# Performance work log

Hardware: AMD Instinct MI355X
Metric: run time of the kernel (lower is better)

The kernel has to match this reference:

```python
import jax, jax.numpy as jnp
import numpy as np

NUM_HEADS = 8
NUM_CONNECTIONS = 4
LOCAL_RADIUS = 1
SPATIAL_SIGMA = 32.0
TEMPORAL_SIGMA = 2.0
SCORER_PATCH_SIZE = (2, 7, 7)  # default used inside compute_proximity_scores
DENSITY_WEIGHT = 1.0
PROXIMITY_WEIGHT = 1.0
NEG = -1e9


def _local_window_mask(N: int, radius: int) -> np.ndarray:
    """Replicates compute_sparse_attention_mask's local-window loop (static)."""
    g = int(np.sqrt(N))
    d = np.arange(-radius, radius + 1)
    dt, dh, dw = np.meshgrid(d, d, d, indexing='ij')
    offsets = (dt * g * g + dh * g + dw).reshape(-1)  # (27,)
    i = np.arange(N)[:, None]
    j = i + offsets[None, :]
    valid = (j >= 0) & (j < N)
    mask = np.zeros((N, N), dtype=bool)
    mask[np.broadcast_to(i, j.shape)[valid], j[valid]] = True
    return mask


def _patch_positions(nT, nH, nW, bt, bh, bw):
    t_idx = np.arange(nT) * bt + bt // 2
    h_idx = np.arange(nH) * bh + bh // 2
    w_idx = np.arange(nW) * bw + bw // 2
    pos = np.stack(np.meshgrid(t_idx, h_idx, w_idx, indexing='ij'), axis=-1)
    return jnp.asarray(pos.reshape(-1, 3), dtype=jnp.float32)  # (N, 3)


def setup_inputs() -> dict:
    key = jax.random.key(0)
    k1, k2, k3 = jax.random.split(key, 3)
    B, T, H, W, C = 1, 4, 28, 28, 256
    x = jax.random.normal(k1, (B, T, H, W, C), dtype=jnp.float32)
    w_qkv = jax.random.normal(k2, (3 * C, C), dtype=jnp.float32) * 0.02
    w_proj = jax.random.normal(k3, (C, C), dtype=jnp.float32) * 0.02
    b_proj = jnp.zeros((C,), dtype=jnp.float32)
    return {"x": x, "w_qkv": w_qkv, "w_proj": w_proj, "b_proj": b_proj,
            "bt": 2, "bh": 7, "bw": 7}


def reference(x, w_qkv, w_proj, b_proj, bt, bh, bw):
    B, T, H, W, C = x.shape
    nT, nH, nW = T // bt, H // bh, W // bw
    N, V = nT * nH * nW, bt * bh * bw
    L = N * V
    hd = C // NUM_HEADS

    # ---- rearrange into patches: b (nt t)(nh h)(nw w) c -> b N V c ----
    patches = x.reshape(B, nT, bt, nH, bh, nW, bw, C)
    patches = patches.transpose(0, 1, 3, 5, 2, 4, 6, 7).reshape(B, N, V, C)

    # ---- density scores (B, N) ----
    dens = jnp.linalg.norm(patches, axis=-1).mean(axis=-1)
    dens = dens / (dens.max(axis=1, keepdims=True) + 1e-8)

    # ---- proximity scores (N, N) ----
    pos = _patch_positions(nT, nH, nW, bt, bh, bw)
    pT, pH, pW = SCORER_PATCH_SIZE
    t_dist = jnp.abs(pos[:, 0:1] - pos[:, 0:1].T) * pT
    h_dist = jnp.abs(pos[:, 1:2] - pos[:, 1:2].T) * pH
    w_dist = jnp.abs(pos[:, 2:3] - pos[:, 2:3].T) * pW
    spatial = jnp.sqrt(h_dist ** 2 + w_dist ** 2)
    prox = jnp.exp(-spatial / SPATIAL_SIGMA) * jnp.exp(-t_dist / TEMPORAL_SIGMA)

    # ---- combined scores (B, N, N) ----
    geo = jnp.sqrt(dens[:, :, None] * dens[:, None, :] + 1e-8)
    scores = DENSITY_WEIGHT * geo + PROXIMITY_WEIGHT * prox[None]

    # ---- sparse attention mask (N, N) ----
    s = scores.mean(0)
    mask = jnp.asarray(_local_window_mask(N, LOCAL_RADIUS))
    k = min(NUM_CONNECTIONS, N - 1)
    s_nodiag = jnp.where(jnp.eye(N, dtype=bool), -jnp.inf, s)
    _, topk_idx = jax.lax.top_k(s_nodiag, k)  # indices: no gradient path
    mask = mask.at[jnp.arange(N)[:, None], topk_idx].set(True)

    # expand block mask to token-level (L, L)
    tmask = jnp.repeat(jnp.repeat(mask, V, axis=0), V, axis=1)

    # ---- block-sparse attention over tokens (dense masked emulation) ----
    tokens = patches.reshape(B, L, C)
    qkv = tokens @ w_qkv.T  # (B, L, 3C)
    q, kk, v = jnp.split(qkv, 3, axis=-1)

    def to_heads(t):
        return t.reshape(B, L, NUM_HEADS, hd).transpose(0, 2, 1, 3)

    q, kk, v = to_heads(q), to_heads(kk), to_heads(v)
    att = jnp.einsum('bhid,bhjd->bhij', q, kk) * (hd ** -0.5)
    att = jnp.where(tmask[None, None], att, NEG)
    att = jax.nn.softmax(att, axis=-1)
    o = jnp.einsum('bhij,bhjd->bhid', att, v)
    o = o.transpose(0, 2, 1, 3).reshape(B, L, C)
    o = o @ w_proj.T + b_proj

    # ---- inverse rearrange back to (B, T, H, W, C) ----
    o = o.reshape(B, nT, nH, nW, bt, bh, bw, C)
    out = o.transpose(0, 1, 4, 2, 5, 3, 6, 7).reshape(B, T, H, W, C)
    return out
```

## Files before the change

### kernel.cpp

```cpp
#include <hip/hip_runtime.h>
#include <hip/hip_bf16.h>
#include <math.h>

#define L_TOK 3136
#define NPATCH 32
#define VTOK 98
#define PADV 128
#define CDIM 256
#define NHEADS 8
#define HD 32

typedef __attribute__((ext_vector_type(8))) short short8;
typedef __attribute__((ext_vector_type(4))) short short4v;
typedef __attribute__((ext_vector_type(4))) float floatx4;

union PU { unsigned u[2]; short4v s; };

static __device__ __forceinline__ unsigned short bf16u(float f) {
    __hip_bfloat16 h = __float2bfloat16(f);
    return *reinterpret_cast<unsigned short*>(&h);
}
static __device__ __forceinline__ float bf16f(unsigned short u) {
    unsigned v = ((unsigned)u) << 16;
    return __uint_as_float(v);
}
static __device__ __forceinline__ void bf16pair(float v, unsigned short& hi, unsigned short& lo) {
    unsigned short h = bf16u(v);
    lo = bf16u(v - bf16f(h));
    hi = h;
}
static __device__ __forceinline__ short8 ldcvt(const float* p) {
    float4 a = *(const float4*)p;
    float4 b = *(const float4*)(p + 4);
    short8 r;
    r[0] = (short)bf16u(a.x); r[1] = (short)bf16u(a.y);
    r[2] = (short)bf16u(a.z); r[3] = (short)bf16u(a.w);
    r[4] = (short)bf16u(b.x); r[5] = (short)bf16u(b.y);
    r[6] = (short)bf16u(b.z); r[7] = (short)bf16u(b.w);
    return r;
}

static __device__ __forceinline__ int token_offset(int l) {
    int pn = l / VTOK, pv = l % VTOK;
    int it = pn >> 4, ih = (pn >> 2) & 3, iw = pn & 3;
    int tt = pv / 49, r2 = pv % 49, hh = r2 / 7, ww = r2 % 7;
    return (((it * 2 + tt) * 28 + ih * 7 + hh) * 28 + iw * 7 + ww) * CDIM;
}

__global__ __launch_bounds__(256) void qkv_density(const float* __restrict__ x,
                                                   const float* __restrict__ wqkv,
                                                   unsigned short* __restrict__ qb,
                                                   unsigned short* __restrict__ kb,
                                                   unsigned short* __restrict__ vt,
                                                   float* __restrict__ dens) {
    __shared__ int rowpn[64];
    __shared__ int rowpv[64];
    __shared__ float wsum[4];
    int tid = threadIdx.x;

    if (blockIdx.y == 12) {
        if (blockIdx.x >= NPATCH) return;
        int n = blockIdx.x;
        int wid = tid >> 6, lane = tid & 63;
        float accn = 0.f;
        for (int v = wid; v < VTOK; v += 4) {
            int off = token_offset(n * VTOK + v);
            float4 xx = *(const float4*)(x + off + lane * 4);
            float ss = xx.x * xx.x + xx.y * xx.y + xx.z * xx.z + xx.w * xx.w;
            #pragma unroll
            for (int o = 32; o > 0; o >>= 1) ss += __shfl_down(ss, o, 64);
            if (lane == 0) accn += sqrtf(ss);
        }
        if (lane == 0) wsum[wid] = accn;
        __syncthreads();
        if (tid == 0) dens[n] = (wsum[0] + wsum[1] + wsum[2] + wsum[3]) * (1.0f / 98.0f);
        return;
    }

    int m0 = blockIdx.x * 64;
    int n0 = blockIdx.y * 64;
    if (tid < 64) {
        int l = m0 + tid;
        rowpn[tid] = l / VTOK;
        rowpv[tid] = l % VTOK;
    }
    __syncthreads();
    const int wave = tid >> 6, lane = tid & 63;
    const int l16 = lane & 15, quad = lane >> 4;
    const int wm = wave & 1, wn = wave >> 1;

    int r0 = m0 + wm * 32 + l16;
    int aoff0 = token_offset(r0);
    int aoff1 = token_offset(r0 + 16);
    int boff0 = (n0 + wn * 32 + l16) * CDIM;
    int boff1 = boff0 + 16 * CDIM;

    const floatx4 zerov = {0.f, 0.f, 0.f, 0.f};
    floatx4 acc[2][2] = {{zerov, zerov}, {zerov, zerov}};
    #pragma unroll
    for (int k0 = 0; k0 < CDIM; k0 += 32) {
        int kk = k0 + quad * 8;
        short8 a0 = ldcvt(x + aoff0 + kk);
        short8 a1 = ldcvt(x + aoff1 + kk);
        short8 b0 = ldcvt(wqkv + boff0 + kk);
        short8 b1 = ldcvt(wqkv + boff1 + kk);
        acc[0][0] = __builtin_amdgcn_mfma_f32_16x16x32_bf16(a0, b0, acc[0][0], 0, 0, 0);
        acc[0][1] = __builtin_amdgcn_mfma_f32_16x16x32_bf16(a0, b1, acc[0][1], 0, 0, 0);
        acc[1][0] = __builtin_amdgcn_mfma_f32_16x16x32_bf16(a1, b0, acc[1][0], 0, 0, 0);
        acc[1][1] = __builtin_amdgcn_mfma_f32_16x16x32_bf16(a1, b1, acc[1][1], 0, 0, 0);
    }

    const float sc = 0.17677669529663689f;
    #pragma unroll
    for (int mt = 0; mt < 2; ++mt) {
        #pragma unroll
        for (int nt = 0; nt < 2; ++nt) {
            int col = n0 + wn * 32 + nt * 16 + l16;
            #pragma unroll
            for (int r = 0; r < 4; ++r) {
                int mrow = wm * 32 + mt * 16 + quad * 4 + r;
                int pn = rowpn[mrow], vv = rowpv[mrow];
                float val = acc[mt][nt][r];
                if (col < 256) {
                    qb[(size_t)(pn * PADV + vv) * CDIM + col] = bf16u(val * sc);
                } else if (col < 512) {
                    kb[(size_t)(pn * PADV + vv) * CDIM + (col - 256)] = bf16u(val);
                } else {
                    vt[(size_t)pn * (CDIM * PADV) + (col - 512) * PADV + vv] = bf16u(val);
                }
            }
        }
    }
}

__global__ __launch_bounds__(256) void attn_mfma(const unsigned short* __restrict__ qb,
                                                 const unsigned short* __restrict__ kb,
                                                 const unsigned short* __restrict__ vt,
                                                 const float* __restrict__ dens,
                                                 unsigned short* __restrict__ ohi,
                                                 unsigned short* __restrict__ olo) {
    __shared__ floatx4 ldsO[4][7][2][64];
    __shared__ float   ldsL[4][7][64];
    const int i = blockIdx.x, h = blockIdx.y;
    const int tid = threadIdx.x;
    const int wave = tid >> 6, lane = tid & 63;
    const int l16 = lane & 15, quad = lane >> 4;

    unsigned maskbits;
    {
        int j = lane & 31;
        float dj = dens[j];
        float m = dj;
        #pragma unroll
        for (int o = 16; o > 0; o >>= 1) m = fmaxf(m, __shfl_xor(m, o, 64));
        float inv = 1.0f / (m + 1e-8f);
        float dni = dens[i] * inv, dnj = dj * inv;
        int it_i = i >> 4, ih_i = (i >> 2) & 3, iw_i = i & 3;
        int it_j = j >> 4, ih_j = (j >> 2) & 3, iw_j = j & 3;
        float t_dist = fabsf((float)(2 * (it_i - it_j))) * 2.0f;
        float h_dist = fabsf((float)(7 * (ih_i - ih_j))) * 7.0f;
        float w_dist = fabsf((float)(7 * (iw_i - iw_j))) * 7.0f;
        float spatial = sqrtf(h_dist * h_dist + w_dist * w_dist);
        float prox = expf(-spatial / 32.0f) * expf(-t_dist / 2.0f);
        float val = (j == i) ? -1e30f : (sqrtf(dni * dnj + 1e-8f) + prox);
        unsigned picked = 0;
        #pragma unroll
        for (int t = 0; t < 4; ++t) {
            float best = val;
            #pragma unroll
            for (int o = 16; o > 0; o >>= 1) best = fmaxf(best, __shfl_xor(best, o, 64));
            unsigned long long b = __ballot(val == best);
            int bj = (__ffsll((long long)b) - 1) & 31;
            picked |= 1u << bj;
            if ((lane & 31) == bj) val = -1e30f;
        }
        int delta = j - i;
        bool inwin = false;
        #pragma unroll
        for (int dt = -1; dt <= 1; ++dt)
            #pragma unroll
            for (int dh = -1; dh <= 1; ++dh)
                #pragma unroll
                for (int dw = -1; dw <= 1; ++dw)
                    inwin = inwin || (delta == dt * 25 + dh * 5 + dw);
        unsigned wmask = (unsigned)(__ballot(inwin) & 0xFFFFFFFFull);
        maskbits = wmask | picked;
    }

    short8 Qf[7];
    #pragma unroll
    for (int t = 0; t < 7; ++t)
        Qf[t] = *(const short8*)(qb + (size_t)(i * PADV + t * 16 + l16) * CDIM + h * HD + quad * 8);

    const floatx4 zerov = {0.f, 0.f, 0.f, 0.f};
    floatx4 O[7][2];
    float lsum[7];
    #pragma unroll
    for (int t = 0; t < 7; ++t) { O[t][0] = zerov; O[t][1] = zerov; lsum[t] = 0.f; }

    unsigned bits = maskbits;
    int rank = 0;
    while (bits) {
        int j = __ffs(bits) - 1;
        bits &= bits - 1;
        if ((rank++ & 3) != wave) continue;
        const unsigned short* kbase = kb + (size_t)(j * PADV) * CDIM + h * HD;
        const unsigned short* vbase = vt + (size_t)j * (CDIM * PADV) + (h * HD) * PADV;
        #pragma unroll
        for (int c = 0; c < 7; ++c) {
            short8 Kf = *(const short8*)(kbase + (c * 16 + l16) * CDIM + quad * 8);
            short4v Vf0 = *(const short4v*)(vbase + l16 * PADV + c * 16 + quad * 4);
            short4v Vf1 = *(const short4v*)(vbase + (16 + l16) * PADV + c * 16 + quad * 4);
            #pragma unroll
            for (int t = 0; t < 7; ++t) {
                floatx4 S = __builtin_amdgcn_mfma_f32_16x16x32_bf16(Kf, Qf[t], zerov, 0, 0, 0);
                unsigned up[4];
                #pragma unroll
                for (int r = 0; r < 4; ++r) {
                    float e = __expf(S[r]);
                    if (c == 6 && !(quad == 0 && r < 2)) e = 0.f;
                    unsigned ue = __float_as_uint(e) & 0xFFFF0000u;
                    up[r] = ue;
                    lsum[t] += __uint_as_float(ue);
                }
                PU pu;
                pu.u[0] = __builtin_amdgcn_perm(up[1], up[0], 0x07060302u);
                pu.u[1] = __builtin_amdgcn_perm(up[3], up[2], 0x07060302u);
                O[t][0] = __builtin_amdgcn_mfma_f32_16x16x16bf16_1k(pu.s, Vf0, O[t][0], 0, 0, 0);
                O[t][1] = __builtin_amdgcn_mfma_f32_16x16x16bf16_1k(pu.s, Vf1, O[t][1], 0, 0, 0);
            }
        }
    }

    #pragma unroll
    for (int t = 0; t < 7; ++t) {
        ldsO[wave][t][0][lane] = O[t][0];
        ldsO[wave][t][1][lane] = O[t][1];
        ldsL[wave][t][lane] = lsum[t];
    }
    __syncthreads();
    for (int u = wave; u < 14; u += 4) {
        int t = u >> 1, half = u & 1;
        floatx4 Os = ldsO[0][t][half][lane] + ldsO[1][t][half][lane]
                   + ldsO[2][t][half][lane] + ldsO[3][t][half][lane];
        float Ls = ldsL[0][t][lane] + ldsL[1][t][lane] + ldsL[2][t][lane] + ldsL[3][t][lane];
        Ls += __shfl_xor(Ls, 16, 64);
        Ls += __shfl_xor(Ls, 32, 64);
        #pragma unroll
        for (int r = 0; r < 4; ++r) {
            int q = t * 16 + quad * 4 + r;
            float lv = __shfl(Ls, quad * 4 + r);
            if (q < VTOK) {
                float invl = 1.0f / lv;
                float v = Os[r] * invl;
                unsigned short hi, lo;
                bf16pair(v, hi, lo);
                size_t base = (size_t)(i * VTOK + q) * CDIM + h * HD + half * 16;
                ohi[base + l16] = hi;
                olo[base + l16] = lo;
            }
        }
    }
}

__global__ __launch_bounds__(256) void proj_gemm(const unsigned short* __restrict__ ohi,
                                                 const unsigned short* __restrict__ olo,
                                                 const float* __restrict__ wproj,
                                                 const float* __restrict__ bp,
                                                 float* __restrict__ out) {
    __shared__ int rowoff[64];
    __shared__ __align__(16) unsigned short Bh[32][264];
    __shared__ __align__(16) unsigned short Bl[32][264];
    int tid = threadIdx.x;
    int m0 = blockIdx.x * 64;
    int n0 = blockIdx.y * 32;
    if (tid < 64) rowoff[tid] = token_offset(m0 + tid);
    #pragma unroll
    for (int rep = 0; rep < 8; ++rep) {
        int flat = rep * 256 + tid;
        int row = flat >> 6;
        int c4 = (flat & 63) * 4;
        float4 v = *(const float4*)(wproj + (size_t)(n0 + row) * CDIM + c4);
        ushort4 uh, ul;
        bf16pair(v.x, uh.x, ul.x); bf16pair(v.y, uh.y, ul.y);
        bf16pair(v.z, uh.z, ul.z); bf16pair(v.w, uh.w, ul.w);
        *(ushort4*)(&Bh[row][c4]) = uh;
        *(ushort4*)(&Bl[row][c4]) = ul;
    }
    __syncthreads();

    const int wave = tid >> 6, lane = tid & 63;
    const int l16 = lane & 15, quad = lane >> 4;

    size_t arow = (size_t)(m0 + wave * 16 + l16) * CDIM + quad * 8;

    const floatx4 zerov = {0.f, 0.f, 0.f, 0.f};
    floatx4 acc[2] = {zerov, zerov};
    #pragma unroll 2
    for (int k0 = 0; k0 < CDIM; k0 += 32) {
        int kk = k0 + quad * 8;
        short8 ah = *(const short8*)(ohi + arow + k0);
        short8 al = *(const short8*)(olo + arow + k0);
        short8 bh0 = *(const short8*)(&Bh[l16][kk]);
        short8 bh1 = *(const short8*)(&Bh[16 + l16][kk]);
        short8 bl0 = *(const short8*)(&Bl[l16][kk]);
        short8 bl1 = *(const short8*)(&Bl[16 + l16][kk]);
        acc[0] = __builtin_amdgcn_mfma_f32_16x16x32_bf16(al, bh0, acc[0], 0, 0, 0);
        acc[0] = __builtin_amdgcn_mfma_f32_16x16x32_bf16(ah, bl0, acc[0], 0, 0, 0);
        acc[0] = __builtin_amdgcn_mfma_f32_16x16x32_bf16(ah, bh0, acc[0], 0, 0, 0);
        acc[1] = __builtin_amdgcn_mfma_f32_16x16x32_bf16(al, bh1, acc[1], 0, 0, 0);
        acc[1] = __builtin_amdgcn_mfma_f32_16x16x32_bf16(ah, bl1, acc[1], 0, 0, 0);
        acc[1] = __builtin_amdgcn_mfma_f32_16x16x32_bf16(ah, bh1, acc[1], 0, 0, 0);
    }

    #pragma unroll
    for (int nt = 0; nt < 2; ++nt) {
        int col = n0 + nt * 16 + l16;
        float bias = bp[col];
        #pragma unroll
        for (int r = 0; r < 4; ++r) {
            int mrow = wave * 16 + quad * 4 + r;
            out[rowoff[mrow] + col] = acc[nt][r] + bias;
        }
    }
}

extern "C" void kernel_launch(void* const* d_in, const int* in_sizes, int n_in,
                              void* d_out, int out_size, void* d_ws, size_t ws_size,
                              hipStream_t stream) {
    const float* x      = (const float*)d_in[0];
    const float* w_qkv  = (const float*)d_in[1];
    const float* w_proj = (const float*)d_in[2];
    const float* b_proj = (const float*)d_in[3];
    float* out = (float*)d_out;

    unsigned short* qb  = (unsigned short*)d_ws;
    unsigned short* kb  = qb  + (size_t)NPATCH * PADV * CDIM;
    unsigned short* vt  = kb  + (size_t)NPATCH * PADV * CDIM;
    unsigned short* ohi = vt  + (size_t)NPATCH * PADV * CDIM;
    unsigned short* olo = ohi + (size_t)L_TOK * CDIM;
    float* dens = (float*)(olo + (size_t)L_TOK * CDIM);

    qkv_density<<<dim3(49, 13), 256, 0, stream>>>(x, w_qkv, qb, kb, vt, dens);
    attn_mfma<<<dim3(NPATCH, NHEADS), 256, 0, stream>>>(qb, kb, vt, dens, ohi, olo);
    proj_gemm<<<dim3(49, 8), 256, 0, stream>>>(ohi, olo, w_proj, b_proj, out);
}
```

Baseline: 119.8 us.

## Fuse attention and projection into one kernel with a software grid barrier

Merges the attention and output-projection kernels into one 256-block launch. A global atomic barrier separates the two phases, and the first 196 blocks then run the projection GEMM with wider 64-column tiles. The goal is to drop one kernel launch and its inter-kernel gap. The barrier needs all 256 blocks to be co-resident, which the large LDS footprint could threaten, and its magic-value reset scheme is fragile across repeated calls. The QKV loop unroll is also reduced to 2.

```diff
diff --git a/kernel.cpp b/kernel.cpp
--- a/kernel.cpp
+++ b/kernel.cpp
@@ -9,6 +9,7 @@
 #define CDIM 256
 #define NHEADS 8
 #define HD 32
+#define BAR_MAGIC 0x5EEDF00Du
 
 typedef __attribute__((ext_vector_type(8))) short short8;
 typedef __attribute__((ext_vector_type(4))) short short4v;
@@ -97,7 +98,7 @@
 
     const floatx4 zerov = {0.f, 0.f, 0.f, 0.f};
     floatx4 acc[2][2] = {{zerov, zerov}, {zerov, zerov}};
-    #pragma unroll
+    #pragma unroll 2
     for (int k0 = 0; k0 < CDIM; k0 += 32) {
         int kk = k0 + quad * 8;
         short8 a0 = ldcvt(x + aoff0 + kk);
@@ -133,194 +134,214 @@
     }
 }
 
-__global__ __launch_bounds__(256) void attn_mfma(const unsigned short* __restrict__ qb,
+#define LDSBYTES 66304
+__global__ __launch_bounds__(256) void attn_proj(const unsigned short* __restrict__ qb,
                                                  const unsigned short* __restrict__ kb,
                                                  const unsigned short* __restrict__ vt,
                                                  const float* __restrict__ dens,
                                                  unsigned short* __restrict__ ohi,
-                                                 unsigned short* __restrict__ olo) {
-    __shared__ floatx4 ldsO[4][7][2][64];
-    __shared__ float   ldsL[4][7][64];
-    const int i = blockIdx.x, h = blockIdx.y;
+                                                 unsigned short* __restrict__ olo,
+                                                 const float* __restrict__ wproj,
+                                                 const float* __restrict__ bp,
+                                                 float* __restrict__ out,
+                                                 unsigned* __restrict__ bar) {
+    __shared__ __align__(16) char ldsbuf[LDSBYTES];
     const int tid = threadIdx.x;
     const int wave = tid >> 6, lane = tid & 63;
     const int l16 = lane & 15, quad = lane >> 4;
 
-    unsigned maskbits;
+    if (blockIdx.x == 0 && tid == 0) {
+        bar[1] = 0u; bar[2] = 0u;
+        __threadfence();
+        atomicExch(&bar[0], BAR_MAGIC);
+    }
+
     {
-        int j = lane & 31;
-        float dj = dens[j];
-        float m = dj;
-        #pragma unroll
-        for (int o = 16; o > 0; o >>= 1) m = fmaxf(m, __shfl_xor(m, o, 64));
-        float inv = 1.0f / (m + 1e-8f);
-        float dni = dens[i] * inv, dnj = dj * inv;
-        int it_i = i >> 4, ih_i = (i >> 2) & 3, iw_i = i & 3;
-        int it_j = j >> 4, ih_j = (j >> 2) & 3, iw_j = j & 3;
-        float t_dist = fabsf((float)(2 * (it_i - it_j))) * 2.0f;
-        float h_dist = fabsf((float)(7 * (ih_i - ih_j))) * 7.0f;
-        float w_dist = fabsf((float)(7 * (iw_i - iw_j))) * 7.0f;
-        float spatial = sqrtf(h_dist * h_dist + w_dist * w_dist);
-        float prox = expf(-spatial / 32.0f) * expf(-t_dist / 2.0f);
-        float val = (j == i) ? -1e30f : (sqrtf(dni * dnj + 1e-8f) + prox);
-        unsigned picked = 0;
-        #pragma unroll
-        for (int t = 0; t < 4; ++t) {
-            float best = val;
-            #pragma unroll
-            for (int o = 16; o > 0; o >>= 1) best = fmaxf(best, __shfl_xor(best, o, 64));
-            unsigned long long b = __ballot(val == best);
-            int bj = (__ffsll((long long)b) - 1) & 31;
-            picked |= 1u << bj;
-            if ((lane & 31) == bj) val = -1e30f;
-        }
-        int delta = j - i;
-        bool inwin = false;
-        #pragma unroll
-        for (int dt = -1; dt <= 1; ++dt)
-            #pragma unroll
-            for (int dh = -1; dh <= 1; ++dh)
+        const int i = blockIdx.x >> 3, h = blockIdx.x & 7;
+        floatx4 (*ldsO)[7][2][64] = (floatx4 (*)[7][2][64])ldsbuf;
+        float   (*ldsL)[7][64]    = (float (*)[7][64])(ldsbuf + 57344);
+
+        unsigned maskbits;
+        {
+            int j = lane & 31;
+            float dj = dens[j];
+            float m = dj;
+            #pragma unroll
+            for (int o = 16; o > 0; o >>= 1) m = fmaxf(m, __shfl_xor(m, o, 64));
+            float inv = 1.0f / (m + 1e-8f);
+            float dni = dens[i] * inv, dnj = dj * inv;
+            int it_i = i >> 4, ih_i = (i >> 2) & 3, iw_i = i & 3;
+            int it_j = j >> 4, ih_j = (j >> 2) & 3, iw_j = j & 3;
+            float t_dist = fabsf((float)(2 * (it_i - it_j))) * 2.0f;
+            float h_dist = fabsf((float)(7 * (ih_i - ih_j))) * 7.0f;
+            float w_dist = fabsf((float)(7 * (iw_i - iw_j))) * 7.0f;
+            float spatial = sqrtf(h_dist * h_dist + w_dist * w_dist);
+            float prox = expf(-spatial / 32.0f) * expf(-t_dist / 2.0f);
+            float val = (j == i) ? -1e30f : (sqrtf(dni * dnj + 1e-8f) + prox);
+            unsigned picked = 0;
+            #pragma unroll
+            for (int t = 0; t < 4; ++t) {
+                float best = val;
                 #pragma unroll
-                for (int dw = -1; dw <= 1; ++dw)
-                    inwin = inwin || (delta == dt * 25 + dh * 5 + dw);
-        unsigned wmask = (unsigned)(__ballot(inwin) & 0xFFFFFFFFull);
-        maskbits = wmask | picked;
-    }
-
-    short8 Qf[7];
-    #pragma unroll
-    for (int t = 0; t < 7; ++t)
-        Qf[t] = *(const short8*)(qb + (size_t)(i * PADV + t * 16 + l16) * CDIM + h * HD + quad * 8);
-
-    const floatx4 zerov = {0.f, 0.f, 0.f, 0.f};
-    floatx4 O[7][2];
-    float lsum[7];
-    #pragma unroll
-    for (int t = 0; t < 7; ++t) { O[t][0] = zerov; O[t][1] = zerov; lsum[t] = 0.f; }
-
-    unsigned bits = maskbits;
-    int rank = 0;
-    while (bits) {
-        int j = __ffs(bits) - 1;
-        bits &= bits - 1;
-        if ((rank++ & 3) != wave) continue;
-        const unsigned short* kbase = kb + (size_t)(j * PADV) * CDIM + h * HD;
-        const unsigned short* vbase = vt + (size_t)j * (CDIM * PADV) + (h * HD) * PADV;
-        #pragma unroll
-        for (int c = 0; c < 7; ++c) {
-            short8 Kf = *(const short8*)(kbase + (c * 16 + l16) * CDIM + quad * 8);
-            short4v Vf0 = *(const short4v*)(vbase + l16 * PADV + c * 16 + quad * 4);
-            short4v Vf1 = *(const short4v*)(vbase + (16 + l16) * PADV + c * 16 + quad * 4);
-            #pragma unroll
-            for (int t = 0; t < 7; ++t) {
-                floatx4 S = __builtin_amdgcn_mfma_f32_16x16x32_bf16(Kf, Qf[t], zerov, 0, 0, 0);
-                unsigned up[4];
+                for (int o = 16; o > 0; o >>= 1) best = fmaxf(best, __shfl_xor(best, o, 64));
+                unsigned long long b = __ballot(val == best);
+                int bj = (__ffsll((long long)b) - 1) & 31;
+                picked |= 1u << bj;
+                if ((lane & 31) == bj) val = -1e30f;
+            }
+            int delta = j - i;
+            bool inwin = false;
+            #pragma unroll
+            for (int dt = -1; dt <= 1; ++dt)
                 #pragma unroll
-                for (int r = 0; r < 4; ++r) {
-                    float e = __expf(S[r]);
-                    if (c == 6 && !(quad == 0 && r < 2)) e = 0.f;
-                    unsigned ue = __float_as_uint(e) & 0xFFFF0000u;
-                    up[r] = ue;
-                    lsum[t] += __uint_as_float(ue);
+                for (int dh = -1; dh <= 1; ++dh)
+                    #pragma unroll
+                    for (int dw = -1; dw <= 1; ++dw)
+                        inwin = inwin || (delta == dt * 25 + dh * 5 + dw);
+            unsigned wmask = (unsigned)(__ballot(inwin) & 0xFFFFFFFFull);
+            maskbits = wmask | picked;
+        }
+
+        short8 Qf[7];
+        #pragma unroll
+        for (int t = 0; t < 7; ++t)
+            Qf[t] = *(const short8*)(qb + (size_t)(i * PADV + t * 16 + l16) * CDIM + h * HD + quad * 8);
+
+        const floatx4 zerov = {0.f, 0.f, 0.f, 0.f};
+        floatx4 O[7][2];
+        float lsum[7];
+        #pragma unroll
+        for (int t = 0; t < 7; ++t) { O[t][0] = zerov; O[t][1] = zerov; lsum[t] = 0.f; }
+
+        unsigned bits = maskbits;
+        int rank = 0;
+        while (bits) {
+            int j = __ffs(bits) - 1;
+            bits &= bits - 1;
+            if ((rank++ & 3) != wave) continue;
+            const unsigned short* kbase = kb + (size_t)(j * PADV) * CDIM + h * HD;
+            const unsigned short* vbase = vt + (size_t)j * (CDIM * PADV) + (h * HD) * PADV;
+            #pragma unroll
+            for (int c = 0; c < 7; ++c) {
+                short8 Kf = *(const short8*)(kbase + (c * 16 + l16) * CDIM + quad * 8);
+                short4v Vf0 = *(const short4v*)(vbase + l16 * PADV + c * 16 + quad * 4);
+                short4v Vf1 = *(const short4v*)(vbase + (16 + l16) * PADV + c * 16 + quad * 4);
+                #pragma unroll
+                for (int t = 0; t < 7; ++t) {
+                    floatx4 S = __builtin_amdgcn_mfma_f32_16x16x32_bf16(Kf, Qf[t], zerov, 0, 0, 0);
+                    unsigned up[4];
+                    #pragma unroll
+                    for (int r = 0; r < 4; ++r) {
+                        float e = __expf(S[r]);
+                        if (c == 6 && !(quad == 0 && r < 2)) e = 0.f;
+                        unsigned ue = __float_as_uint(e) & 0xFFFF0000u;
+                        up[r] = ue;
+                        lsum[t] += __uint_as_float(ue);
+                    }
+                    PU pu;
+                    pu.u[0] = __builtin_amdgcn_perm(up[1], up[0], 0x07060302u);
+                    pu.u[1] = __builtin_amdgcn_perm(up[3], up[2], 0x07060302u);
+                    O[t][0] = __builtin_amdgcn_mfma_f32_16x16x16bf16_1k(pu.s, Vf0, O[t][0], 0, 0, 0);
+                    O[t][1] = __builtin_amdgcn_mfma_f32_16x16x16bf16_1k(pu.s, Vf1, O[t][1], 0, 0, 0);
                 }
-                PU pu;
-                pu.u[0] = __builtin_amdgcn_perm(up[1], up[0], 0x07060302u);
-                pu.u[1] = __builtin_amdgcn_perm(up[3], up[2], 0x07060302u);
-                O[t][0] = __builtin_amdgcn_mfma_f32_16x16x16bf16_1k(pu.s, Vf0, O[t][0], 0, 0, 0);
-                O[t][1] = __builtin_amdgcn_mfma_f32_16x16x16bf16_1k(pu.s, Vf1, O[t][1], 0, 0, 0);
-            }
-        }
-    }
-
-    #pragma unroll
-    for (int t = 0; t < 7; ++t) {
-        ldsO[wave][t][0][lane] = O[t][0];
-        ldsO[wave][t][1][lane] = O[t][1];
-        ldsL[wave][t][lane] = lsum[t];
-    }
+            }
+        }
+
+        #pragma unroll
+        for (int t = 0; t < 7; ++t) {
+            ldsO[wave][t][0][lane] = O[t][0];
+            ldsO[wave][t][1][lane] = O[t][1];
+            ldsL[wave][t][lane] = lsum[t];
+        }
+        __syncthreads();
+        for (int u = wave; u < 14; u += 4) {
+            int t = u >> 1, half = u & 1;
+            floatx4 Os = ldsO[0][t][half][lane] + ldsO[1][t][half][lane]
+                       + ldsO[2][t][half][lane] + ldsO[3][t][half][lane];
+            float Ls = ldsL[0][t][lane] + ldsL[1][t][lane] + ldsL[2][t][lane] + ldsL[3][t][lane];
+            Ls += __shfl_xor(Ls, 16, 64);
+            Ls += __shfl_xor(Ls, 32, 64);
+            #pragma unroll
+            for (int r = 0; r < 4; ++r) {
+                int q = t * 16 + quad * 4 + r;
+                float lv = __shfl(Ls, quad * 4 + r);
+                if (q < VTOK) {
+                    float invl = 1.0f / lv;
+                    float v = Os[r] * invl;
+                    unsigned short hi, lo;
+                    bf16pair(v, hi, lo);
+                    size_t base = (size_t)(i * VTOK + q) * CDIM + h * HD + half * 16;
+                    ohi[base + l16] = hi;
+                    olo[base + l16] = lo;
+                }
+            }
+        }
+    }
+
+    __threadfence();
     __syncthreads();
-    for (int u = wave; u < 14; u += 4) {
-        int t = u >> 1, half = u & 1;
-        floatx4 Os = ldsO[0][t][half][lane] + ldsO[1][t][half][lane]
-                   + ldsO[2][t][half][lane] + ldsO[3][t][half][lane];
-        float Ls = ldsL[0][t][lane] + ldsL[1][t][lane] + ldsL[2][t][lane] + ldsL[3][t][lane];
-        Ls += __shfl_xor(Ls, 16, 64);
-        Ls += __shfl_xor(Ls, 32, 64);
-        #pragma unroll
-        for (int r = 0; r < 4; ++r) {
-            int q = t * 16 + quad * 4 + r;
-            float lv = __shfl(Ls, quad * 4 + r);
-            if (q < VTOK) {
-                float invl = 1.0f / lv;
-                float v = Os[r] * invl;
-                unsigned short hi, lo;
-                bf16pair(v, hi, lo);
-                size_t base = (size_t)(i * VTOK + q) * CDIM + h * HD + half * 16;
-                ohi[base + l16] = hi;
-                olo[base + l16] = lo;
-            }
-        }
-    }
-}
-
-__global__ __launch_bounds__(256) void proj_gemm(const unsigned short* __restrict__ ohi,
-                                                 const unsigned short* __restrict__ olo,
-                                                 const float* __restrict__ wproj,
-                                                 const float* __restrict__ bp,
-                                                 float* __restrict__ out) {
-    __shared__ int rowoff[64];
-    __shared__ __align__(16) unsigned short Bh[32][264];
-    __shared__ __align__(16) unsigned short Bl[32][264];
-    int tid = threadIdx.x;
-    int m0 = blockIdx.x * 64;
-    int n0 = blockIdx.y * 32;
-    if (tid < 64) rowoff[tid] = token_offset(m0 + tid);
-    #pragma unroll
-    for (int rep = 0; rep < 8; ++rep) {
-        int flat = rep * 256 + tid;
-        int row = flat >> 6;
-        int c4 = (flat & 63) * 4;
-        float4 v = *(const float4*)(wproj + (size_t)(n0 + row) * CDIM + c4);
-        ushort4 uh, ul;
-        bf16pair(v.x, uh.x, ul.x); bf16pair(v.y, uh.y, ul.y);
-        bf16pair(v.z, uh.z, ul.z); bf16pair(v.w, uh.w, ul.w);
-        *(ushort4*)(&Bh[row][c4]) = uh;
-        *(ushort4*)(&Bl[row][c4]) = ul;
+    if (tid == 0) {
+        while (atomicAdd(&bar[0], 0u) != BAR_MAGIC) __builtin_amdgcn_s_sleep(2);
+        unsigned a = atomicAdd(&bar[1], 1u);
+        if (a == (unsigned)(gridDim.x - 1)) {
+            atomicExch(&bar[2], 1u);
+        } else {
+            while (atomicAdd(&bar[2], 0u) == 0u) __builtin_amdgcn_s_sleep(2);
+        }
     }
     __syncthreads();
-
-    const int wave = tid >> 6, lane = tid & 63;
-    const int l16 = lane & 15, quad = lane >> 4;
-
-    size_t arow = (size_t)(m0 + wave * 16 + l16) * CDIM + quad * 8;
-
-    const floatx4 zerov = {0.f, 0.f, 0.f, 0.f};
-    floatx4 acc[2] = {zerov, zerov};
-    #pragma unroll 2
-    for (int k0 = 0; k0 < CDIM; k0 += 32) {
-        int kk = k0 + quad * 8;
-        short8 ah = *(const short8*)(ohi + arow + k0);
-        short8 al = *(const short8*)(olo + arow + k0);
-        short8 bh0 = *(const short8*)(&Bh[l16][kk]);
-        short8 bh1 = *(const short8*)(&Bh[16 + l16][kk]);
-        short8 bl0 = *(const short8*)(&Bl[l16][kk]);
-        short8 bl1 = *(const short8*)(&Bl[16 + l16][kk]);
-        acc[0] = __builtin_amdgcn_mfma_f32_16x16x32_bf16(al, bh0, acc[0], 0, 0, 0);
-        acc[0] = __builtin_amdgcn_mfma_f32_16x16x32_bf16(ah, bl0, acc[0], 0, 0, 0);
-        acc[0] = __builtin_amdgcn_mfma_f32_16x16x32_bf16(ah, bh0, acc[0], 0, 0, 0);
-        acc[1] = __builtin_amdgcn_mfma_f32_16x16x32_bf16(al, bh1, acc[1], 0, 0, 0);
-        acc[1] = __builtin_amdgcn_mfma_f32_16x16x32_bf16(ah, bl1, acc[1], 0, 0, 0);
-        acc[1] = __builtin_amdgcn_mfma_f32_16x16x32_bf16(ah, bh1, acc[1], 0, 0, 0);
-    }
-
-    #pragma unroll
-    for (int nt = 0; nt < 2; ++nt) {
-        int col = n0 + nt * 16 + l16;
-        float bias = bp[col];
-        #pragma unroll
-        for (int r = 0; r < 4; ++r) {
-            int mrow = wave * 16 + quad * 4 + r;
-            out[rowoff[mrow] + col] = acc[nt][r] + bias;
+    __threadfence();
+
+    if (blockIdx.x >= 196) return;
+    {
+        int m0 = (blockIdx.x % 49) * 64;
+        int n0 = (blockIdx.x / 49) * 64;
+        int* rowoff = (int*)ldsbuf;
+        unsigned short (*Bh)[258] = (unsigned short (*)[258])(ldsbuf + 256);
+        unsigned short (*Bl)[258] = (unsigned short (*)[258])(ldsbuf + 256 + 33024);
+
+        if (tid < 64) rowoff[tid] = token_offset(m0 + tid);
+        #pragma unroll
+        for (int rep = 0; rep < 16; ++rep) {
+            int flat = rep * 256 + tid;
+            int row = flat >> 6;
+            int c4 = (flat & 63) * 4;
+            float4 v = *(const float4*)(wproj + (size_t)(n0 + row) * CDIM + c4);
+            ushort4 uh, ul;
+            bf16pair(v.x, uh.x, ul.x); bf16pair(v.y, uh.y, ul.y);
+            bf16pair(v.z, uh.z, ul.z); bf16pair(v.w, uh.w, ul.w);
+            *(ushort4*)(&Bh[row][c4]) = uh;
+            *(ushort4*)(&Bl[row][c4]) = ul;
+        }
+        __syncthreads();
+
+        size_t arow = (size_t)(m0 + wave * 16 + l16) * CDIM + quad * 8;
+        const floatx4 zerov = {0.f, 0.f, 0.f, 0.f};
+        floatx4 acc[4] = {zerov, zerov, zerov, zerov};
+        #pragma unroll 2
+        for (int k0 = 0; k0 < CDIM; k0 += 32) {
+            int kk = k0 + quad * 8;
+            short8 ah = *(const short8*)(ohi + arow + k0);
+            short8 al = *(const short8*)(olo + arow + k0);
+            #pragma unroll
+            for (int nt = 0; nt < 4; ++nt) {
+                short8 bh = *(const short8*)(&Bh[nt * 16 + l16][kk]);
+                short8 bl = *(const short8*)(&Bl[nt * 16 + l16][kk]);
+                acc[nt] = __builtin_amdgcn_mfma_f32_16x16x32_bf16(al, bh, acc[nt], 0, 0, 0);
+                acc[nt] = __builtin_amdgcn_mfma_f32_16x16x32_bf16(ah, bl, acc[nt], 0, 0, 0);
+                acc[nt] = __builtin_amdgcn_mfma_f32_16x16x32_bf16(ah, bh, acc[nt], 0, 0, 0);
+            }
+        }
+
+        #pragma unroll
+        for (int nt = 0; nt < 4; ++nt) {
+            int col = n0 + nt * 16 + l16;
+            float bias = bp[col];
+            #pragma unroll
+            for (int r = 0; r < 4; ++r) {
+                int mrow = wave * 16 + quad * 4 + r;
+                out[rowoff[mrow] + col] = acc[nt][r] + bias;
+            }
         }
     }
 }
@@ -340,8 +361,8 @@
     unsigned short* ohi = vt  + (size_t)NPATCH * PADV * CDIM;
     unsigned short* olo = ohi + (size_t)L_TOK * CDIM;
     float* dens = (float*)(olo + (size_t)L_TOK * CDIM);
+    unsigned* bar = (unsigned*)(dens + NPATCH);
 
     qkv_density<<<dim3(49, 13), 256, 0, stream>>>(x, w_qkv, qb, kb, vt, dens);
-    attn_mfma<<<dim3(NPATCH, NHEADS), 256, 0, stream>>>(qb, kb, vt, dens, ohi, olo);
-    proj_gemm<<<dim3(49, 8), 256, 0, stream>>>(ohi, olo, w_proj, b_proj, out);
-}
+    attn_proj<<<256, 256, 0, stream>>>(qb, kb, vt, dens, ohi, olo, w_proj, b_proj, out, bar);
+}
```

Measured after the change: 178.4 us. 48.9% more time.

## Stage QKV output through LDS, store V row-major, use 8 waves in attention

Applied to the files above, without the earlier changes.

The QKV epilogue now writes bf16 results into an LDS tile and then emits coalesced 16-byte row stores for Q, K and V. V is kept row-major instead of transposed, which removes the strided scatter of the V^T writes. The attention kernel reads V with per-row 32-bit loads and repacks them into MFMA operands with perm instructions. It also runs 8 waves per block instead of 4, splitting the neighbour patches across more waves and adding a two-stage LDS reduction. The costs are extra V load instructions and more register pressure per block, and the QKV k-loop is now only partly unrolled.

```diff
diff --git a/kernel.cpp b/kernel.cpp
--- a/kernel.cpp
+++ b/kernel.cpp
@@ -51,11 +51,12 @@
                                                    const float* __restrict__ wqkv,
                                                    unsigned short* __restrict__ qb,
                                                    unsigned short* __restrict__ kb,
-                                                   unsigned short* __restrict__ vt,
+                                                   unsigned short* __restrict__ vb,
                                                    float* __restrict__ dens) {
     __shared__ int rowpn[64];
     __shared__ int rowpv[64];
     __shared__ float wsum[4];
+    __shared__ __align__(16) unsigned short Ct[64][72];
     int tid = threadIdx.x;
 
     if (blockIdx.y == 12) {
@@ -97,7 +98,7 @@
 
     const floatx4 zerov = {0.f, 0.f, 0.f, 0.f};
     floatx4 acc[2][2] = {{zerov, zerov}, {zerov, zerov}};
-    #pragma unroll
+    #pragma unroll 2
     for (int k0 = 0; k0 < CDIM; k0 += 32) {
         int kk = k0 + quad * 8;
         short8 a0 = ldcvt(x + aoff0 + kk);
@@ -110,32 +111,31 @@
         acc[1][1] = __builtin_amdgcn_mfma_f32_16x16x32_bf16(a1, b1, acc[1][1], 0, 0, 0);
     }
 
-    const float sc = 0.17677669529663689f;
-    #pragma unroll
-    for (int mt = 0; mt < 2; ++mt) {
-        #pragma unroll
-        for (int nt = 0; nt < 2; ++nt) {
-            int col = n0 + wn * 32 + nt * 16 + l16;
-            #pragma unroll
-            for (int r = 0; r < 4; ++r) {
-                int mrow = wm * 32 + mt * 16 + quad * 4 + r;
-                int pn = rowpn[mrow], vv = rowpv[mrow];
-                float val = acc[mt][nt][r];
-                if (col < 256) {
-                    qb[(size_t)(pn * PADV + vv) * CDIM + col] = bf16u(val * sc);
-                } else if (col < 512) {
-                    kb[(size_t)(pn * PADV + vv) * CDIM + (col - 256)] = bf16u(val);
-                } else {
-                    vt[(size_t)pn * (CDIM * PADV) + (col - 512) * PADV + vv] = bf16u(val);
-                }
-            }
-        }
-    }
-}
-
-__global__ __launch_bounds__(256) void attn_mfma(const unsigned short* __restrict__ qb,
+    const int ytype = blockIdx.y >> 2;
+    const float sc = (ytype == 0) ? 0.17677669529663689f : 1.0f;
+    #pragma unroll
+    for (int mt = 0; mt < 2; ++mt)
+        #pragma unroll
+        for (int nt = 0; nt < 2; ++nt)
+            #pragma unroll
+            for (int r = 0; r < 4; ++r)
+                Ct[wm * 32 + mt * 16 + quad * 4 + r][wn * 32 + nt * 16 + l16] =
+                    bf16u(acc[mt][nt][r] * sc);
+    __syncthreads();
+    unsigned short* ob = (ytype == 0) ? qb : (ytype == 1) ? kb : vb;
+    int nlocal0 = (blockIdx.y & 3) * 64;
+    #pragma unroll
+    for (int it = 0; it < 2; ++it) {
+        int idx = it * 256 + tid;
+        int row = idx >> 3, chunk = idx & 7;
+        short8 cv = *(const short8*)(&Ct[row][chunk * 8]);
+        *(short8*)(ob + (size_t)(rowpn[row] * PADV + rowpv[row]) * CDIM + nlocal0 + chunk * 8) = cv;
+    }
+}
+
+__global__ __launch_bounds__(512) void attn_mfma(const unsigned short* __restrict__ qb,
                                                  const unsigned short* __restrict__ kb,
-                                                 const unsigned short* __restrict__ vt,
+                                                 const unsigned short* __restrict__ vb,
                                                  const float* __restrict__ dens,
                                                  unsigned short* __restrict__ ohi,
                                                  unsigned short* __restrict__ olo) {
@@ -203,14 +203,21 @@
     while (bits) {
         int j = __ffs(bits) - 1;
         bits &= bits - 1;
-        if ((rank++ & 3) != wave) continue;
+        if ((rank++ & 7) != wave) continue;
         const unsigned short* kbase = kb + (size_t)(j * PADV) * CDIM + h * HD;
-        const unsigned short* vbase = vt + (size_t)j * (CDIM * PADV) + (h * HD) * PADV;
+        const unsigned short* vbase = vb + (size_t)(j * PADV) * CDIM + h * HD + 2 * l16;
         #pragma unroll
         for (int c = 0; c < 7; ++c) {
             short8 Kf = *(const short8*)(kbase + (c * 16 + l16) * CDIM + quad * 8);
-            short4v Vf0 = *(const short4v*)(vbase + l16 * PADV + c * 16 + quad * 4);
-            short4v Vf1 = *(const short4v*)(vbase + (16 + l16) * PADV + c * 16 + quad * 4);
+            unsigned w0 = *(const unsigned*)(vbase + (c * 16 + quad * 4 + 0) * CDIM);
+            unsigned w1 = *(const unsigned*)(vbase + (c * 16 + quad * 4 + 1) * CDIM);
+            unsigned w2 = *(const unsigned*)(vbase + (c * 16 + quad * 4 + 2) * CDIM);
+            unsigned w3 = *(const unsigned*)(vbase + (c * 16 + quad * 4 + 3) * CDIM);
+            PU vf0, vf1;
+            vf0.u[0] = __builtin_amdgcn_perm(w1, w0, 0x05040100u);
+            vf0.u[1] = __builtin_amdgcn_perm(w3, w2, 0x05040100u);
+            vf1.u[0] = __builtin_amdgcn_perm(w1, w0, 0x07060302u);
+            vf1.u[1] = __builtin_amdgcn_perm(w3, w2, 0x07060302u);
             #pragma unroll
             for (int t = 0; t < 7; ++t) {
                 floatx4 S = __builtin_amdgcn_mfma_f32_16x16x32_bf16(Kf, Qf[t], zerov, 0, 0, 0);
@@ -226,23 +233,40 @@
                 PU pu;
                 pu.u[0] = __builtin_amdgcn_perm(up[1], up[0], 0x07060302u);
                 pu.u[1] = __builtin_amdgcn_perm(up[3], up[2], 0x07060302u);
-                O[t][0] = __builtin_amdgcn_mfma_f32_16x16x16bf16_1k(pu.s, Vf0, O[t][0], 0, 0, 0);
-                O[t][1] = __builtin_amdgcn_mfma_f32_16x16x16bf16_1k(pu.s, Vf1, O[t][1], 0, 0, 0);
+                O[t][0] = __builtin_amdgcn_mfma_f32_16x16x16bf16_1k(pu.s, vf0.s, O[t][0], 0, 0, 0);
+                O[t][1] = __builtin_amdgcn_mfma_f32_16x16x16bf16_1k(pu.s, vf1.s, O[t][1], 0, 0, 0);
             }
         }
     }
 
-    #pragma unroll
-    for (int t = 0; t < 7; ++t) {
-        ldsO[wave][t][0][lane] = O[t][0];
-        ldsO[wave][t][1][lane] = O[t][1];
-        ldsL[wave][t][lane] = lsum[t];
-    }
-    __syncthreads();
-    for (int u = wave; u < 14; u += 4) {
-        int t = u >> 1, half = u & 1;
-        floatx4 Os = ldsO[0][t][half][lane] + ldsO[1][t][half][lane]
-                   + ldsO[2][t][half][lane] + ldsO[3][t][half][lane];
+    if (wave >= 4) {
+        int s = wave - 4;
+        #pragma unroll
+        for (int t = 0; t < 7; ++t) {
+            ldsO[s][t][0][lane] = O[t][0];
+            ldsO[s][t][1][lane] = O[t][1];
+            ldsL[s][t][lane] = lsum[t];
+        }
+    }
+    __syncthreads();
+    if (wave < 4) {
+        #pragma unroll
+        for (int t = 0; t < 7; ++t) {
+            O[t][0] += ldsO[wave][t][0][lane];
+            O[t][1] += ldsO[wave][t][1][lane];
+            lsum[t] += ldsL[wave][t][lane];
+            ldsO[wave][t][0][lane] = O[t][0];
+            ldsO[wave][t][1][lane] = O[t][1];
+            ldsL[wave][t][lane] = lsum[t];
+        }
+    }
+    __syncthreads();
+    if (wave < 7) {
+        int t = wave;
+        floatx4 Os0 = ldsO[0][t][0][lane] + ldsO[1][t][0][lane]
+                    + ldsO[2][t][0][lane] + ldsO[3][t][0][lane];
+        floatx4 Os1 = ldsO[0][t][1][lane] + ldsO[1][t][1][lane]
+                    + ldsO[2][t][1][lane] + ldsO[3][t][1][lane];
         float Ls = ldsL[0][t][lane] + ldsL[1][t][lane] + ldsL[2][t][lane] + ldsL[3][t][lane];
         Ls += __shfl_xor(Ls, 16, 64);
         Ls += __shfl_xor(Ls, 32, 64);
@@ -252,12 +276,13 @@
             float lv = __shfl(Ls, quad * 4 + r);
             if (q < VTOK) {
                 float invl = 1.0f / lv;
-                float v = Os[r] * invl;
-                unsigned short hi, lo;
-                bf16pair(v, hi, lo);
-                size_t base = (size_t)(i * VTOK + q) * CDIM + h * HD + half * 16;
-                ohi[base + l16] = hi;
-                olo[base + l16] = lo;
+                float v0 = Os0[r] * invl, v1 = Os1[r] * invl;
+                unsigned short h0, g0, h1, g1;
+                bf16pair(v0, h0, g0);
+                bf16pair(v1, h1, g1);
+                size_t base = (size_t)(i * VTOK + q) * CDIM + h * HD + 2 * l16;
+                *(unsigned*)(ohi + base) = (unsigned)h0 | ((unsigned)h1 << 16);
+                *(unsigned*)(olo + base) = (unsigned)g0 | ((unsigned)g1 << 16);
             }
         }
     }
@@ -336,12 +361,12 @@
 
     unsigned short* qb  = (unsigned short*)d_ws;
     unsigned short* kb  = qb  + (size_t)NPATCH * PADV * CDIM;
-    unsigned short* vt  = kb  + (size_t)NPATCH * PADV * CDIM;
-    unsigned short* ohi = vt  + (size_t)NPATCH * PADV * CDIM;
+    unsigned short* vb  = kb  + (size_t)NPATCH * PADV * CDIM;
+    unsigned short* ohi = vb  + (size_t)NPATCH * PADV * CDIM;
     unsigned short* olo = ohi + (size_t)L_TOK * CDIM;
     float* dens = (float*)(olo + (size_t)L_TOK * CDIM);
 
-    qkv_density<<<dim3(49, 13), 256, 0, stream>>>(x, w_qkv, qb, kb, vt, dens);
-    attn_mfma<<<dim3(NPATCH, NHEADS), 256, 0, stream>>>(qb, kb, vt, dens, ohi, olo);
+    qkv_density<<<dim3(49, 13), 256, 0, stream>>>(x, w_qkv, qb, kb, vb, dens);
+    attn_mfma<<<dim3(NPATCH, NHEADS), 512, 0, stream>>>(qb, kb, vb, dens, ohi, olo);
     proj_gemm<<<dim3(49, 8), 256, 0, stream>>>(ohi, olo, w_proj, b_proj, out);
 }
```

After: 119.9 us. Within noise of the previous version (+0.1%).
